# Optimization experiments

Measured on AMD Instinct MI355X. Metric: run time of the kernel, lower is better.

## Reference

```python
import jax, jax.numpy as jnp
import numpy as np


def entmax15(x):
    # Exact entmax with alpha=1.5 (Peters et al. 2019), applied along last dim.
    x = x / 2.0
    x = x - jnp.max(x, axis=-1, keepdims=True)

    d = x.shape[-1]
    xsrt = -jnp.sort(-x, axis=-1)                      # descending sort
    rho = jnp.arange(1, d + 1, dtype=x.dtype)          # [d]
    mean = jnp.cumsum(xsrt, axis=-1) / rho             # running mean
    mean_sq = jnp.cumsum(xsrt * xsrt, axis=-1) / rho   # running mean of squares
    ss = rho * (mean_sq - mean * mean)
    delta = (1.0 - ss) / rho
    delta_nz = jnp.maximum(delta, 0.0)
    tau = mean - jnp.sqrt(delta_nz)                    # candidate thresholds

    support_size = jnp.sum((tau <= xsrt).astype(jnp.int32), axis=-1, keepdims=True)
    tau_star = jnp.take_along_axis(tau, support_size - 1, axis=-1)

    y = jnp.maximum(x - tau_star, 0.0)
    return y * y


def setup_inputs() -> dict:
    key = jax.random.key(0)
    x = jax.random.normal(key, (8, 16, 1024, 1024), dtype=jnp.float32)
    return {"x": x}


def reference(x) -> jnp.ndarray:
    return entmax15(x)
```

## Files before the change

### kernel.cpp

```cpp
#include <hip/hip_runtime.h>


constexpr int D = 1024;
constexpr int WAVES_PER_BLOCK = 4;

__global__ __launch_bounds__(256) void entmax15_kernel(const float* __restrict__ x,
                                                       float* __restrict__ y,
                                                       int nrows) {
    const int wave = threadIdx.x >> 6;
    const int lane = threadIdx.x & 63;
    const int row  = blockIdx.x * WAVES_PER_BLOCK + wave;
    if (row >= nrows) return;

    const float4* xr = (const float4*)(x + (size_t)row * D);
    float4*       yr = (float4*)(y + (size_t)row * D);

    float4 v[4];
#pragma unroll
    for (int j = 0; j < 4; ++j) v[j] = xr[lane + 64 * j];

    float m = -3.4e38f;
#pragma unroll
    for (int j = 0; j < 4; ++j) {
        v[j].x *= 0.5f; v[j].y *= 0.5f; v[j].z *= 0.5f; v[j].w *= 0.5f;
        m = fmaxf(m, fmaxf(fmaxf(v[j].x, v[j].y), fmaxf(v[j].z, v[j].w)));
    }
#pragma unroll
    for (int off = 32; off >= 1; off >>= 1) m = fmaxf(m, __shfl_xor(m, off));

#pragma unroll
    for (int j = 0; j < 4; ++j) { v[j].x -= m; v[j].y -= m; v[j].z -= m; v[j].w -= m; }

    float tau = -1.0f;
    for (int it = 0; it < 50; ++it) {
        float s1 = 0.f, s2 = 0.f;
#pragma unroll
        for (int j = 0; j < 4; ++j) {
            float t;
            t = fmaxf(v[j].x - tau, 0.f); s1 += t; s2 = fmaf(t, t, s2);
            t = fmaxf(v[j].y - tau, 0.f); s1 += t; s2 = fmaf(t, t, s2);
            t = fmaxf(v[j].z - tau, 0.f); s1 += t; s2 = fmaf(t, t, s2);
            t = fmaxf(v[j].w - tau, 0.f); s1 += t; s2 = fmaf(t, t, s2);
        }
#pragma unroll
        for (int off = 32; off >= 1; off >>= 1) {
            s1 += __shfl_xor(s1, off);
            s2 += __shfl_xor(s2, off);
        }
        float diff = s2 - 1.0f;
        if (diff <= 1e-7f) break;
        float tnew = tau + diff / (2.0f * s1);
        if (tnew == tau) break;
        tau = tnew;
    }

#pragma unroll
    for (int j = 0; j < 4; ++j) {
        float4 o; float t;
        t = fmaxf(v[j].x - tau, 0.f); o.x = t * t;
        t = fmaxf(v[j].y - tau, 0.f); o.y = t * t;
        t = fmaxf(v[j].z - tau, 0.f); o.z = t * t;
        t = fmaxf(v[j].w - tau, 0.f); o.w = t * t;
        yr[lane + 64 * j] = o;
    }
}

extern "C" void kernel_launch(void* const* d_in, const int* in_sizes, int n_in,
                              void* d_out, int out_size, void* d_ws, size_t ws_size,
                              hipStream_t stream) {
    const float* x = (const float*)d_in[0];
    float*       y = (float*)d_out;
    const int nrows = in_sizes[0] / D;
    const int blocks = (nrows + WAVES_PER_BLOCK - 1) / WAVES_PER_BLOCK;
    entmax15_kernel<<<blocks, 256, 0, stream>>>(x, y, nrows);
}
```

Before: 825.4 us.

## Use exact quadratic step for tau solve, fold scaling, nontemporal I/O

Replaces the Newton iteration on tau with a step that solves the local quadratic exactly, using the active-element count gathered via ballot/popcount. This should converge in far fewer iterations, so the cap drops from 50 to 10 and the stopping tolerance is loosened. The x/2 scale and max shift are folded into an fma inside each iteration, removing separate passes over the values. Loads and stores become nontemporal. Risks: a small accuracy change from the looser tolerance and iteration cap, and extra ballot instructions added to every iteration.

```diff
diff --git a/kernel.cpp b/kernel.cpp
--- a/kernel.cpp
+++ b/kernel.cpp
@@ -3,6 +3,8 @@
 
 constexpr int D = 1024;
 constexpr int WAVES_PER_BLOCK = 4;
+
+using f32x4 = __attribute__((ext_vector_type(4))) float;
 
 __global__ __launch_bounds__(256) void entmax15_kernel(const float* __restrict__ x,
                                                        float* __restrict__ y,
@@ -12,56 +14,61 @@
     const int row  = blockIdx.x * WAVES_PER_BLOCK + wave;
     if (row >= nrows) return;
 
-    const float4* xr = (const float4*)(x + (size_t)row * D);
-    float4*       yr = (float4*)(y + (size_t)row * D);
+    const f32x4* xr = (const f32x4*)(x + (size_t)row * D);
+    f32x4*       yr = (f32x4*)(y + (size_t)row * D);
 
-    float4 v[4];
+    f32x4 v[4];
 #pragma unroll
-    for (int j = 0; j < 4; ++j) v[j] = xr[lane + 64 * j];
+    for (int j = 0; j < 4; ++j) v[j] = __builtin_nontemporal_load(xr + lane + 64 * j);
 
     float m = -3.4e38f;
 #pragma unroll
-    for (int j = 0; j < 4; ++j) {
-        v[j].x *= 0.5f; v[j].y *= 0.5f; v[j].z *= 0.5f; v[j].w *= 0.5f;
+    for (int j = 0; j < 4; ++j)
         m = fmaxf(m, fmaxf(fmaxf(v[j].x, v[j].y), fmaxf(v[j].z, v[j].w)));
-    }
 #pragma unroll
     for (int off = 32; off >= 1; off >>= 1) m = fmaxf(m, __shfl_xor(m, off));
 
-#pragma unroll
-    for (int j = 0; j < 4; ++j) { v[j].x -= m; v[j].y -= m; v[j].z -= m; v[j].w -= m; }
-
-    float tau = -1.0f;
-    for (int it = 0; it < 50; ++it) {
+    float tau = fmaf(0.5f, m, -1.0f);
+#pragma unroll 1
+    for (int it = 0; it < 10; ++it) {
         float s1 = 0.f, s2 = 0.f;
+        int kc = 0;
 #pragma unroll
         for (int j = 0; j < 4; ++j) {
             float t;
-            t = fmaxf(v[j].x - tau, 0.f); s1 += t; s2 = fmaf(t, t, s2);
-            t = fmaxf(v[j].y - tau, 0.f); s1 += t; s2 = fmaf(t, t, s2);
-            t = fmaxf(v[j].z - tau, 0.f); s1 += t; s2 = fmaf(t, t, s2);
-            t = fmaxf(v[j].w - tau, 0.f); s1 += t; s2 = fmaf(t, t, s2);
+            t = fmaxf(fmaf(0.5f, v[j].x, -tau), 0.f); s1 += t; s2 = fmaf(t, t, s2);
+            kc += (int)__popcll(__ballot(t > 0.f));
+            t = fmaxf(fmaf(0.5f, v[j].y, -tau), 0.f); s1 += t; s2 = fmaf(t, t, s2);
+            kc += (int)__popcll(__ballot(t > 0.f));
+            t = fmaxf(fmaf(0.5f, v[j].z, -tau), 0.f); s1 += t; s2 = fmaf(t, t, s2);
+            kc += (int)__popcll(__ballot(t > 0.f));
+            t = fmaxf(fmaf(0.5f, v[j].w, -tau), 0.f); s1 += t; s2 = fmaf(t, t, s2);
+            kc += (int)__popcll(__ballot(t > 0.f));
         }
 #pragma unroll
         for (int off = 32; off >= 1; off >>= 1) {
             s1 += __shfl_xor(s1, off);
             s2 += __shfl_xor(s2, off);
         }
-        float diff = s2 - 1.0f;
-        if (diff <= 1e-7f) break;
-        float tnew = tau + diff / (2.0f * s1);
+        const float diff = s2 - 1.0f;
+        if (fabsf(diff) <= 4e-6f) break;
+        const float K    = (float)kc;
+        const float disc = fmaf(-K, diff, s1 * s1);
+        const float delta = (disc > 0.f) ? (diff / (s1 + __builtin_sqrtf(disc)))
+                                         : (diff / (2.0f * s1));
+        const float tnew = tau + delta;
         if (tnew == tau) break;
         tau = tnew;
     }
 
 #pragma unroll
     for (int j = 0; j < 4; ++j) {
-        float4 o; float t;
-        t = fmaxf(v[j].x - tau, 0.f); o.x = t * t;
-        t = fmaxf(v[j].y - tau, 0.f); o.y = t * t;
-        t = fmaxf(v[j].z - tau, 0.f); o.z = t * t;
-        t = fmaxf(v[j].w - tau, 0.f); o.w = t * t;
-        yr[lane + 64 * j] = o;
+        f32x4 o; float t;
+        t = fmaxf(fmaf(0.5f, v[j].x, -tau), 0.f); o.x = t * t;
+        t = fmaxf(fmaf(0.5f, v[j].y, -tau), 0.f); o.y = t * t;
+        t = fmaxf(fmaf(0.5f, v[j].z, -tau), 0.f); o.z = t * t;
+        t = fmaxf(fmaf(0.5f, v[j].w, -tau), 0.f); o.w = t * t;
+        __builtin_nontemporal_store(o, yr + lane + 64 * j);
     }
 }
 
```

After: 807.0 us. 2.2% less time.
